# Performance work log

Measured on AMD Instinct MI355X. Metric: run time of the kernel, lower is better.

The kernel has to match this reference:

```python
import jax, jax.numpy as jnp
import numpy as np

EMBED = 1024
HEADS = 16
HEAD_DIM = EMBED // HEADS
HIDDEN = 4096
EPS = 1e-5


def setup_inputs() -> dict:
    key = jax.random.key(0)
    ks = jax.random.split(key, 12)
    s = 0.02
    inp = {
        "x": jax.random.normal(ks[0], (2, 2048, EMBED), dtype=jnp.float32),
        "ln1_scale": jnp.ones((EMBED,), jnp.float32),
        "ln1_shift": jnp.zeros((EMBED,), jnp.float32),
        "ln2_scale": jnp.ones((EMBED,), jnp.float32),
        "ln2_shift": jnp.zeros((EMBED,), jnp.float32),
        "wq": jax.random.normal(ks[1], (EMBED, EMBED), jnp.float32) * s,
        "bq": jnp.zeros((EMBED,), jnp.float32),
        "wk": jax.random.normal(ks[2], (EMBED, EMBED), jnp.float32) * s,
        "bk": jnp.zeros((EMBED,), jnp.float32),
        "wv": jax.random.normal(ks[3], (EMBED, EMBED), jnp.float32) * s,
        "bv": jnp.zeros((EMBED,), jnp.float32),
        "wo": jax.random.normal(ks[4], (EMBED, EMBED), jnp.float32) * s,
        "bo": jnp.zeros((EMBED,), jnp.float32),
        "w1": jax.random.normal(ks[5], (EMBED, HIDDEN), jnp.float32) * s,
        "b1": jnp.zeros((HIDDEN,), jnp.float32),
        "w2": jax.random.normal(ks[6], (HIDDEN, EMBED), jnp.float32) * s,
        "b2": jnp.zeros((EMBED,), jnp.float32),
    }
    return inp


def _layernorm(x, scale, shift):
    mean = jnp.mean(x, axis=-1, keepdims=True)
    var = jnp.var(x, axis=-1, keepdims=True)
    return scale * (x - mean) * jax.lax.rsqrt(var + EPS) + shift


def _block(x, ln1_scale, ln1_shift, ln2_scale, ln2_shift,
           wq, bq, wk, bk, wv, bv, wo, bo, w1, b1, w2, b2):
    B, S, D = x.shape
    h = _layernorm(x, ln1_scale, ln1_shift)
    q = (h @ wq + bq).reshape(B, S, HEADS, HEAD_DIM).transpose(0, 2, 1, 3)
    k = (h @ wk + bk).reshape(B, S, HEADS, HEAD_DIM).transpose(0, 2, 1, 3)
    v = (h @ wv + bv).reshape(B, S, HEADS, HEAD_DIM).transpose(0, 2, 1, 3)
    # [B,H,S,S] eager attention scores, matching the reference exactly
    scores = jnp.einsum("bhqd,bhkd->bhqk", q, k) * (HEAD_DIM ** -0.5)
    causal = jnp.tril(jnp.ones((S, S), dtype=bool))
    scores = jnp.where(causal, scores, -jnp.inf)
    attn = jax.nn.softmax(scores, axis=-1)
    ctx = jnp.einsum("bhqk,bhkd->bhqd", attn, v)
    ctx = ctx.transpose(0, 2, 1, 3).reshape(B, S, D)
    x = x + (ctx @ wo + bo)
    h = _layernorm(x, ln2_scale, ln2_shift)
    h = jax.nn.gelu(h @ w1 + b1, approximate=False)
    x = x + (h @ w2 + b2)
    return x


def reference(x, ln1_scale, ln1_shift, ln2_scale, ln2_shift,
              wq, bq, wk, bk, wv, bv, wo, bo, w1, b1, w2, b2):
    return _block(x, ln1_scale, ln1_shift, ln2_scale, ln2_shift,
                  wq, bq, wk, bk, wv, bv, wo, bo, w1, b1, w2, b2)
```

## Files before the change

kernel.cpp:

```cpp
#include <hip/hip_runtime.h>


typedef __bf16 bf16x8_t __attribute__((ext_vector_type(8)));
typedef float f32x4_t __attribute__((ext_vector_type(4)));
typedef unsigned short u16x8 __attribute__((ext_vector_type(8)));

__device__ __forceinline__ unsigned short f2b(float f) {
    unsigned int u = __builtin_bit_cast(unsigned int, f);
    u += 0x7fffu + ((u >> 16) & 1u);
    return (unsigned short)(u >> 16);
}
__device__ __forceinline__ bf16x8_t as_bf(u16x8 v) {
    return __builtin_bit_cast(bf16x8_t, v);
}
__device__ __forceinline__ void store_out(float* p, float v) { *p = v; }
__device__ __forceinline__ void store_out(unsigned short* p, float v) { *p = f2b(v); }

__device__ __forceinline__ void glds16(const unsigned short* g, unsigned short* l) {
    __builtin_amdgcn_global_load_lds(
        (const __attribute__((address_space(1))) unsigned int*)g,
        (__attribute__((address_space(3))) unsigned int*)l, 16, 0, 0);
}

template <int N>
__device__ __forceinline__ void wait_vm() {
    asm volatile("s_waitcnt vmcnt(%0)" ::"i"(N) : "memory");
}

__global__ __launch_bounds__(256) void transpose_cast(
    const float* __restrict__ src, unsigned short* __restrict__ dst,
    int K, int N) {
    __shared__ float tile[32][33];
    const int k0 = blockIdx.x * 32, n0 = blockIdx.y * 32;
    const int c = threadIdx.x & 31, r8 = threadIdx.x >> 5;
#pragma unroll
    for (int i = 0; i < 4; i++) {
        const int r = r8 + i * 8;
        tile[r][c] = src[(size_t)(k0 + r) * N + n0 + c];
    }
    __syncthreads();
#pragma unroll
    for (int i = 0; i < 4; i++) {
        const int rr = r8 + i * 8;
        dst[(size_t)(n0 + rr) * K + k0 + c] = f2b(tile[c][rr]);
    }
}

__global__ __launch_bounds__(256) void transpose_cast4(
    const float* __restrict__ s0, const float* __restrict__ s1,
    const float* __restrict__ s2, const float* __restrict__ s3,
    unsigned short* __restrict__ wqkvt, unsigned short* __restrict__ wot) {
    __shared__ float tile[32][33];
    const int z = blockIdx.z;
    const float* src = (z == 0) ? s0 : (z == 1) ? s1 : (z == 2) ? s2 : s3;
    unsigned short* dst = (z < 3) ? wqkvt + ((size_t)z << 20) : wot;
    const int k0 = blockIdx.x * 32, n0 = blockIdx.y * 32;
    const int c = threadIdx.x & 31, r8 = threadIdx.x >> 5;
#pragma unroll
    for (int i = 0; i < 4; i++) {
        const int r = r8 + i * 8;
        tile[r][c] = src[(size_t)(k0 + r) * 1024 + n0 + c];
    }
    __syncthreads();
#pragma unroll
    for (int i = 0; i < 4; i++) {
        const int rr = r8 + i * 8;
        dst[(size_t)(n0 + rr) * 1024 + k0 + c] = f2b(tile[c][rr]);
    }
}

__global__ __launch_bounds__(256) void vtrans_kernel(
    const unsigned short* __restrict__ src, unsigned short* __restrict__ dst) {
    __shared__ unsigned short tile[32][34];
    const int s0 = blockIdx.x * 32, hd0 = blockIdx.y * 32, b = blockIdx.z;
    const int c = threadIdx.x & 31, r8 = threadIdx.x >> 5;
#pragma unroll
    for (int i = 0; i < 4; i++) {
        const int r = r8 + i * 8;
        tile[r][c] = src[(size_t)(b * 2048 + s0 + r) * 3072 + hd0 + c];
    }
    __syncthreads();
#pragma unroll
    for (int i = 0; i < 4; i++) {
        const int rr = r8 + i * 8;
        dst[(size_t)(b * 1024 + hd0 + rr) * 2048 + s0 + c] = tile[c][rr];
    }
}

__global__ __launch_bounds__(256) void ln_kernel(
    const float* __restrict__ X,
    const float* __restrict__ scale,
    const float* __restrict__ shift,
    unsigned short* __restrict__ Hout) {
    const int tok = blockIdx.x;
    const int tid = threadIdx.x;
    const size_t base = (size_t)tok * 1024 + tid * 4;
    float4 xv = *(const float4*)(X + base);
    float f[4] = {xv.x, xv.y, xv.z, xv.w};
    float s = 0.f, s2 = 0.f;
#pragma unroll
    for (int i = 0; i < 4; i++) { s += f[i]; s2 += f[i] * f[i]; }
#pragma unroll
    for (int off = 32; off >= 1; off >>= 1) {
        s += __shfl_down(s, off);
        s2 += __shfl_down(s2, off);
    }
    __shared__ float red[8];
    const int wv = tid >> 6;
    if ((tid & 63) == 0) { red[wv] = s; red[4 + wv] = s2; }
    __syncthreads();
    s = red[0] + red[1] + red[2] + red[3];
    s2 = red[4] + red[5] + red[6] + red[7];
    const float mean = s * (1.f / 1024.f);
    const float var = s2 * (1.f / 1024.f) - mean * mean;
    const float rstd = rsqrtf(var + 1e-5f);
    const float4 sc = *(const float4*)(scale + tid * 4);
    const float4 sh = *(const float4*)(shift + tid * 4);
    unsigned short ov[4];
    ov[0] = f2b((f[0] - mean) * rstd * sc.x + sh.x);
    ov[1] = f2b((f[1] - mean) * rstd * sc.y + sh.y);
    ov[2] = f2b((f[2] - mean) * rstd * sc.z + sh.z);
    ov[3] = f2b((f[3] - mean) * rstd * sc.w + sh.w);
    *(unsigned long long*)(Hout + base) = *(unsigned long long*)ov;
}

template <int BN, int EPI, typename OutT>
__global__ __launch_bounds__(256) void gemm_kernel(
    const unsigned short* __restrict__ A, const unsigned short* __restrict__ Bt,
    const float* __restrict__ bp0, const float* __restrict__ bp1,
    const float* __restrict__ bp2, const float* __restrict__ bp3,
    const float* __restrict__ res, OutT* __restrict__ C, int M, int N, int K) {
    constexpr int BSUB = BN / 16;
    constexpr int JF = BN / 32;
    __shared__ __align__(16) unsigned short As[2][8 * 512];
    __shared__ __align__(16) unsigned short Bs[2][BSUB * 512];
    const int tid = threadIdx.x;
    const int w = tid >> 6, lane = tid & 63;
    const int quad = lane >> 4, l16 = lane & 15;
    const int bm = blockIdx.x * 128, bn = blockIdx.y * BN;
    const int wm = (w & 1) * 64, wn = (w >> 1) * (BN / 2);

    f32x4_t acc[4][JF];
#pragma unroll
    for (int i = 0; i < 4; i++)
#pragma unroll
        for (int j = 0; j < JF; j++) acc[i][j] = f32x4_t{0.f, 0.f, 0.f, 0.f};

    const unsigned short* Abase = A + (size_t)(bm + l16) * K + quad * 8;
    const unsigned short* Bbase = Bt + (size_t)(bn + l16) * K + quad * 8;

    {
        for (int s = w; s < 8; s += 4)
            glds16(Abase + (size_t)s * 16 * K, &As[0][s * 512]);
        for (int s = w; s < BSUB; s += 4)
            glds16(Bbase + (size_t)s * 16 * K, &Bs[0][s * 512]);
    }
    __syncthreads();

    int buf = 0;
    for (int k0 = 0; k0 < K; k0 += 32) {
        if (k0 + 32 < K) {
            const int kn = k0 + 32;
            for (int s = w; s < 8; s += 4)
                glds16(Abase + (size_t)s * 16 * K + kn, &As[buf ^ 1][s * 512]);
            for (int s = w; s < BSUB; s += 4)
                glds16(Bbase + (size_t)s * 16 * K + kn, &Bs[buf ^ 1][s * 512]);
        }
        bf16x8_t af[4], bfv[JF];
#pragma unroll
        for (int i = 0; i < 4; i++)
            af[i] = as_bf(*(const u16x8*)&As[buf][((wm >> 4) + i) * 512 + lane * 8]);
#pragma unroll
        for (int j = 0; j < JF; j++)
            bfv[j] = as_bf(*(const u16x8*)&Bs[buf][((wn >> 4) + j) * 512 + lane * 8]);
#pragma unroll
        for (int i = 0; i < 4; i++)
#pragma unroll
            for (int j = 0; j < JF; j++)
                acc[i][j] = __builtin_amdgcn_mfma_f32_16x16x32_bf16(af[i], bfv[j], acc[i][j], 0, 0, 0);
        __syncthreads();
        buf ^= 1;
    }

#pragma unroll
    for (int i = 0; i < 4; i++) {
        const int row = bm + wm + i * 16 + quad * 4;
#pragma unroll
        for (int j = 0; j < JF; j++) {
            const int col = bn + wn + j * 16 + l16;
            const int sel = col >> 10;
            const float* bp = (sel == 0) ? bp0 : (sel == 1) ? bp1 : (sel == 2) ? bp2 : bp3;
            const float bv = bp[col & 1023];
#pragma unroll
            for (int r = 0; r < 4; r++) {
                float v = acc[i][j][r] + bv;
                if (EPI == 1) v += res[(size_t)(row + r) * N + col];
                if (EPI == 2) v = 0.5f * v * (1.f + erff(v * 0.70710678118f));
                store_out(&C[(size_t)(row + r) * N + col], v);
            }
        }
    }
}

template <int EPI, typename OutT>
__global__ __launch_bounds__(512, 2) void gemm_pipe256(
    const unsigned short* __restrict__ A, const unsigned short* __restrict__ Bt,
    const float* __restrict__ bp0, const float* __restrict__ bp1,
    const float* __restrict__ bp2, const float* __restrict__ bp3,
    OutT* __restrict__ C, int M, int N, int K) {
    constexpr int D = 3, NBUF = 4;
    __shared__ __align__(16) unsigned short As[NBUF][16 * 512];
    __shared__ __align__(16) unsigned short Bs[NBUF][16 * 512];
    const int tid = threadIdx.x;
    const int w = tid >> 6, lane = tid & 63;
    const int quad = lane >> 4, l16 = lane & 15;
    const int bm = blockIdx.x * 256, bn = blockIdx.y * 256;
    const int wm = (w & 1) * 128, wn = (w >> 1) * 64;

    f32x4_t acc[8][4];
#pragma unroll
    for (int i = 0; i < 8; i++)
#pragma unroll
        for (int j = 0; j < 4; j++) acc[i][j] = f32x4_t{0.f, 0.f, 0.f, 0.f};

    const unsigned short* Abase = A + (size_t)(bm + l16) * K + quad * 8;
    const unsigned short* Bbase = Bt + (size_t)(bn + l16) * K + quad * 8;

    auto stage = [&](int kt, int bufi) {
        const int kn = kt * 32;
        const int s0 = w * 2, s1 = w * 2 + 1;
        glds16(Abase + (size_t)s0 * 16 * K + kn, &As[bufi][s0 * 512]);
        glds16(Abase + (size_t)s1 * 16 * K + kn, &As[bufi][s1 * 512]);
        glds16(Bbase + (size_t)s0 * 16 * K + kn, &Bs[bufi][s0 * 512]);
        glds16(Bbase + (size_t)s1 * 16 * K + kn, &Bs[bufi][s1 * 512]);
    };
    auto compute = [&](int bufi) {
        bf16x8_t af[8], bfv[4];
#pragma unroll
        for (int i = 0; i < 8; i++)
            af[i] = as_bf(*(const u16x8*)&As[bufi][((wm >> 4) + i) * 512 + lane * 8]);
#pragma unroll
        for (int j = 0; j < 4; j++)
            bfv[j] = as_bf(*(const u16x8*)&Bs[bufi][((wn >> 4) + j) * 512 + lane * 8]);
#pragma unroll
        for (int i = 0; i < 8; i++)
#pragma unroll
            for (int j = 0; j < 4; j++)
                acc[i][j] = __builtin_amdgcn_mfma_f32_16x16x32_bf16(af[i], bfv[j], acc[i][j], 0, 0, 0);
    };

    const int NT = K >> 5;
#pragma unroll
    for (int t = 0; t < D; ++t) stage(t, t);

    int buf = 0, sbuf = D;
    for (int t = 0; t < NT - D; ++t) {
        wait_vm<8>();
        __builtin_amdgcn_s_barrier();
        __builtin_amdgcn_sched_barrier(0);
        stage(t + D, sbuf);
        sbuf = (sbuf + 1) & 3;
        compute(buf);
        buf = (buf + 1) & 3;
    }
    wait_vm<8>(); __builtin_amdgcn_s_barrier(); __builtin_amdgcn_sched_barrier(0);
    compute(buf); buf = (buf + 1) & 3;
    wait_vm<4>(); __builtin_amdgcn_s_barrier(); __builtin_amdgcn_sched_barrier(0);
    compute(buf); buf = (buf + 1) & 3;
    wait_vm<0>(); __builtin_amdgcn_s_barrier(); __builtin_amdgcn_sched_barrier(0);
    compute(buf);

#pragma unroll
    for (int i = 0; i < 8; i++) {
        const int row = bm + wm + i * 16 + quad * 4;
#pragma unroll
        for (int j = 0; j < 4; j++) {
            const int col = bn + wn + j * 16 + l16;
            const int sel = col >> 10;
            const float* bp = (sel == 0) ? bp0 : (sel == 1) ? bp1 : (sel == 2) ? bp2 : bp3;
            const float bv = bp[col & 1023];
#pragma unroll
            for (int r = 0; r < 4; r++) {
                float v = acc[i][j][r] + bv;
                if (EPI == 2) v = 0.5f * v * (1.f + erff(v * 0.70710678118f));
                store_out(&C[(size_t)(row + r) * N + col], v);
            }
        }
    }
}

#define LP 68

__global__ __launch_bounds__(256, 3) void attn_kernel(
    const unsigned short* __restrict__ Q, const unsigned short* __restrict__ K,
    const unsigned short* __restrict__ Vt, unsigned short* __restrict__ O,
    int ld) {
    __shared__ __align__(16) unsigned short Ks[2][8 * 512];
    __shared__ __align__(16) unsigned short Vs[2][8 * 512];
    __shared__ __align__(16) unsigned short Ps[4][32 * LP];
    const int tid = threadIdx.x;
    const int w = tid >> 6, lane = tid & 63;
    const int quad = lane >> 4, l16 = lane & 15;
    const int hh = blockIdx.x >> 1, bb = blockIdx.x & 1;
    const int y = blockIdx.y;
    const int qb = (y >= 8) ? (y - 8) : (15 - y);
    const int q0 = qb * 128;
    const int tmax = 2 * qb + 1;
    const size_t seqbase = (size_t)bb * 2048;
    const int hoff = hh * 64;
    const unsigned short* vtb = Vt + (size_t)(bb * 16 + hh) * 64 * 2048;
    const float cs = 0.18033688f;

    bf16x8_t qf[2][2];
#pragma unroll
    for (int i = 0; i < 2; i++) {
        const unsigned short* qr = Q + (seqbase + q0 + i * 64 + w * 16 + l16) * ld + hoff;
        qf[i][0] = as_bf(*(const u16x8*)(qr + quad * 8));
        qf[i][1] = as_bf(*(const u16x8*)(qr + 32 + quad * 8));
    }

    f32x4_t o[2][4];
#pragma unroll
    for (int i = 0; i < 2; i++)
#pragma unroll
        for (int jd = 0; jd < 4; jd++) o[i][jd] = f32x4_t{0.f, 0.f, 0.f, 0.f};
    float ls[2][4] = {{0.f, 0.f, 0.f, 0.f}, {0.f, 0.f, 0.f, 0.f}};

    auto stage = [&](int t, int buf) {
        for (int s = w; s < 16; s += 4) {
            if (s < 8) {
                const unsigned short* src =
                    K + (seqbase + t * 64 + (s >> 1) * 16 + l16) * ld + hoff + (s & 1) * 32 + quad * 8;
                glds16(src, &Ks[buf][s * 512]);
            } else {
                const int v = s - 8;
                const unsigned short* src =
                    vtb + (size_t)((v >> 1) * 16 + l16) * 2048 + t * 64 + (v & 1) * 32 + quad * 8;
                glds16(src, &Vs[buf][v * 512]);
            }
        }
    };

    stage(0, 0);
    __syncthreads();

    int buf = 0;
    for (int t = 0; t <= tmax; ++t) {
        if (t < tmax) stage(t + 1, buf ^ 1);

        bf16x8_t kf[4][2], vf[4][2];
#pragma unroll
        for (int jn = 0; jn < 4; jn++) {
            kf[jn][0] = as_bf(*(const u16x8*)&Ks[buf][(jn * 2 + 0) * 512 + lane * 8]);
            kf[jn][1] = as_bf(*(const u16x8*)&Ks[buf][(jn * 2 + 1) * 512 + lane * 8]);
            vf[jn][0] = as_bf(*(const u16x8*)&Vs[buf][(jn * 2 + 0) * 512 + lane * 8]);
            vf[jn][1] = as_bf(*(const u16x8*)&Vs[buf][(jn * 2 + 1) * 512 + lane * 8]);
        }

#pragma unroll
        for (int i = 0; i < 2; i++) {
            if (i == 0 && t > 2 * qb) continue;
            const bool diag = (t == 2 * qb + i);
#pragma unroll
            for (int jn = 0; jn < 4; jn++) {
                f32x4_t z = f32x4_t{0.f, 0.f, 0.f, 0.f};
                z = __builtin_amdgcn_mfma_f32_16x16x32_bf16(qf[i][0], kf[jn][0], z, 0, 0, 0);
                z = __builtin_amdgcn_mfma_f32_16x16x32_bf16(qf[i][1], kf[jn][1], z, 0, 0, 0);
#pragma unroll
                for (int r = 0; r < 4; r++) {
                    float p = exp2f(fminf(z[r] * cs, 60.f));
                    if (diag) {
                        const int col = t * 64 + jn * 16 + l16;
                        const int row = q0 + i * 64 + w * 16 + quad * 4 + r;
                        p = (col <= row) ? p : 0.f;
                    }
                    ls[i][r] += p;
                    Ps[w][(i * 16 + quad * 4 + r) * LP + jn * 16 + l16] = f2b(p);
                }
            }
        }

#pragma unroll
        for (int i = 0; i < 2; i++) {
            if (i == 0 && t > 2 * qb) continue;
            const bf16x8_t pf0 = as_bf(*(const u16x8*)&Ps[w][(i * 16 + l16) * LP + quad * 8]);
            const bf16x8_t pf1 = as_bf(*(const u16x8*)&Ps[w][(i * 16 + l16) * LP + 32 + quad * 8]);
#pragma unroll
            for (int jd = 0; jd < 4; jd++) {
                o[i][jd] = __builtin_amdgcn_mfma_f32_16x16x32_bf16(pf0, vf[jd][0], o[i][jd], 0, 0, 0);
                o[i][jd] = __builtin_amdgcn_mfma_f32_16x16x32_bf16(pf1, vf[jd][1], o[i][jd], 0, 0, 0);
            }
        }
        __syncthreads();
        buf ^= 1;
    }

#pragma unroll
    for (int i = 0; i < 2; i++)
#pragma unroll
        for (int r = 0; r < 4; r++) {
            float s = ls[i][r];
            s += __shfl_xor(s, 1);
            s += __shfl_xor(s, 2);
            s += __shfl_xor(s, 4);
            s += __shfl_xor(s, 8);
            const float inv = 1.f / s;
            const size_t row = seqbase + q0 + i * 64 + w * 16 + quad * 4 + r;
#pragma unroll
            for (int jd = 0; jd < 4; jd++)
                O[row * 1024 + hoff + jd * 16 + l16] = f2b(o[i][jd][r] * inv);
        }
}

extern "C" void kernel_launch(void* const* d_in, const int* in_sizes, int n_in,
                              void* d_out, int out_size, void* d_ws, size_t ws_size,
                              hipStream_t stream) {
    const float* x = (const float*)d_in[0];
    const float* ln1s = (const float*)d_in[1];
    const float* ln1b = (const float*)d_in[2];
    const float* ln2s = (const float*)d_in[3];
    const float* ln2b = (const float*)d_in[4];
    const float* wq = (const float*)d_in[5];
    const float* bq = (const float*)d_in[6];
    const float* wk = (const float*)d_in[7];
    const float* bk = (const float*)d_in[8];
    const float* wv = (const float*)d_in[9];
    const float* bv = (const float*)d_in[10];
    const float* wo = (const float*)d_in[11];
    const float* bo = (const float*)d_in[12];
    const float* w1 = (const float*)d_in[13];
    const float* b1 = (const float*)d_in[14];
    const float* w2 = (const float*)d_in[15];
    const float* b2 = (const float*)d_in[16];
    float* out = (float*)d_out;

    char* ws = (char*)d_ws;
    const size_t MB = 1u << 20;
    unsigned short* wqkvt = (unsigned short*)(ws + 0 * MB);
    unsigned short* wot   = (unsigned short*)(ws + 6 * MB);
    unsigned short* w1t   = (unsigned short*)(ws + 8 * MB);
    unsigned short* w2t   = (unsigned short*)(ws + 16 * MB);
    unsigned short* h     = (unsigned short*)(ws + 24 * MB);
    unsigned short* vt    = (unsigned short*)(ws + 24 * MB);
    unsigned short* qkv   = (unsigned short*)(ws + 32 * MB);
    unsigned short* ctx   = (unsigned short*)(ws + 56 * MB);
    unsigned short* h2    = (unsigned short*)(ws + 24 * MB);
    float*          x1    = (float*)(ws + 64 * MB);
    unsigned short* g     = (unsigned short*)(ws + 32 * MB);

    const dim3 blk(256);

    transpose_cast4<<<dim3(32, 32, 4), blk, 0, stream>>>(wq, wk, wv, wo, wqkvt, wot);
    transpose_cast<<<dim3(32, 128), blk, 0, stream>>>(w1, w1t, 1024, 4096);
    transpose_cast<<<dim3(128, 32), blk, 0, stream>>>(w2, w2t, 4096, 1024);

    ln_kernel<<<4096, blk, 0, stream>>>(x, ln1s, ln1b, h);
    gemm_pipe256<0, unsigned short><<<dim3(16, 12), dim3(512), 0, stream>>>(
        h, wqkvt, bq, bk, bv, bv, qkv, 4096, 3072, 1024);
    vtrans_kernel<<<dim3(64, 32, 2), blk, 0, stream>>>(qkv + 2048, vt);
    attn_kernel<<<dim3(32, 16), blk, 0, stream>>>(qkv, qkv + 1024, vt, ctx, 3072);
    gemm_kernel<64, 1, float><<<dim3(32, 16), blk, 0, stream>>>(
        ctx, wot, bo, bo, bo, bo, x, x1, 4096, 1024, 1024);
    ln_kernel<<<4096, blk, 0, stream>>>(x1, ln2s, ln2b, h2);
    gemm_pipe256<2, unsigned short><<<dim3(16, 16), dim3(512), 0, stream>>>(
        h2, w1t, b1, b1 + 1024, b1 + 2048, b1 + 3072, g, 4096, 4096, 1024);
    gemm_kernel<64, 1, float><<<dim3(32, 16), blk, 0, stream>>>(
        g, w2t, b2, b2, b2, b2, x1, out, 4096, 1024, 4096);
}
```

Measured before the change: 486.9 us.

## Replace N=1024 GEMMs with split-K 256-tile pipeline using atomic accumulation

```diff
diff --git a/kernel.cpp b/kernel.cpp
--- a/kernel.cpp
+++ b/kernel.cpp
@@ -124,82 +124,16 @@
     *(unsigned long long*)(Hout + base) = *(unsigned long long*)ov;
 }
 
-template <int BN, int EPI, typename OutT>
-__global__ __launch_bounds__(256) void gemm_kernel(
-    const unsigned short* __restrict__ A, const unsigned short* __restrict__ Bt,
-    const float* __restrict__ bp0, const float* __restrict__ bp1,
-    const float* __restrict__ bp2, const float* __restrict__ bp3,
-    const float* __restrict__ res, OutT* __restrict__ C, int M, int N, int K) {
-    constexpr int BSUB = BN / 16;
-    constexpr int JF = BN / 32;
-    __shared__ __align__(16) unsigned short As[2][8 * 512];
-    __shared__ __align__(16) unsigned short Bs[2][BSUB * 512];
-    const int tid = threadIdx.x;
-    const int w = tid >> 6, lane = tid & 63;
-    const int quad = lane >> 4, l16 = lane & 15;
-    const int bm = blockIdx.x * 128, bn = blockIdx.y * BN;
-    const int wm = (w & 1) * 64, wn = (w >> 1) * (BN / 2);
-
-    f32x4_t acc[4][JF];
-#pragma unroll
-    for (int i = 0; i < 4; i++)
-#pragma unroll
-        for (int j = 0; j < JF; j++) acc[i][j] = f32x4_t{0.f, 0.f, 0.f, 0.f};
-
-    const unsigned short* Abase = A + (size_t)(bm + l16) * K + quad * 8;
-    const unsigned short* Bbase = Bt + (size_t)(bn + l16) * K + quad * 8;
-
-    {
-        for (int s = w; s < 8; s += 4)
-            glds16(Abase + (size_t)s * 16 * K, &As[0][s * 512]);
-        for (int s = w; s < BSUB; s += 4)
-            glds16(Bbase + (size_t)s * 16 * K, &Bs[0][s * 512]);
-    }
-    __syncthreads();
-
-    int buf = 0;
-    for (int k0 = 0; k0 < K; k0 += 32) {
-        if (k0 + 32 < K) {
-            const int kn = k0 + 32;
-            for (int s = w; s < 8; s += 4)
-                glds16(Abase + (size_t)s * 16 * K + kn, &As[buf ^ 1][s * 512]);
-            for (int s = w; s < BSUB; s += 4)
-                glds16(Bbase + (size_t)s * 16 * K + kn, &Bs[buf ^ 1][s * 512]);
-        }
-        bf16x8_t af[4], bfv[JF];
-#pragma unroll
-        for (int i = 0; i < 4; i++)
-            af[i] = as_bf(*(const u16x8*)&As[buf][((wm >> 4) + i) * 512 + lane * 8]);
-#pragma unroll
-        for (int j = 0; j < JF; j++)
-            bfv[j] = as_bf(*(const u16x8*)&Bs[buf][((wn >> 4) + j) * 512 + lane * 8]);
-#pragma unroll
-        for (int i = 0; i < 4; i++)
-#pragma unroll
-            for (int j = 0; j < JF; j++)
-                acc[i][j] = __builtin_amdgcn_mfma_f32_16x16x32_bf16(af[i], bfv[j], acc[i][j], 0, 0, 0);
-        __syncthreads();
-        buf ^= 1;
-    }
-
-#pragma unroll
-    for (int i = 0; i < 4; i++) {
-        const int row = bm + wm + i * 16 + quad * 4;
-#pragma unroll
-        for (int j = 0; j < JF; j++) {
-            const int col = bn + wn + j * 16 + l16;
-            const int sel = col >> 10;
-            const float* bp = (sel == 0) ? bp0 : (sel == 1) ? bp1 : (sel == 2) ? bp2 : bp3;
-            const float bv = bp[col & 1023];
-#pragma unroll
-            for (int r = 0; r < 4; r++) {
-                float v = acc[i][j][r] + bv;
-                if (EPI == 1) v += res[(size_t)(row + r) * N + col];
-                if (EPI == 2) v = 0.5f * v * (1.f + erff(v * 0.70710678118f));
-                store_out(&C[(size_t)(row + r) * N + col], v);
-            }
-        }
-    }
+__global__ __launch_bounds__(256) void bias_res_init(
+    const float* __restrict__ res, const float* __restrict__ bias,
+    float* __restrict__ out) {
+    const size_t i = (size_t)blockIdx.x * 256 + threadIdx.x;
+    const int col4 = (int)(i & 255);
+    const float4 r = ((const float4*)res)[i];
+    const float4 b = ((const float4*)bias)[col4];
+    float4 o;
+    o.x = r.x + b.x; o.y = r.y + b.y; o.z = r.z + b.z; o.w = r.w + b.w;
+    ((float4*)out)[i] = o;
 }
 
 template <int EPI, typename OutT>
@@ -207,7 +141,7 @@
     const unsigned short* __restrict__ A, const unsigned short* __restrict__ Bt,
     const float* __restrict__ bp0, const float* __restrict__ bp1,
     const float* __restrict__ bp2, const float* __restrict__ bp3,
-    OutT* __restrict__ C, int M, int N, int K) {
+    OutT* __restrict__ C, int M, int N, int K, int Ko) {
     constexpr int D = 3, NBUF = 4;
     __shared__ __align__(16) unsigned short As[NBUF][16 * 512];
     __shared__ __align__(16) unsigned short Bs[NBUF][16 * 512];
@@ -215,6 +149,7 @@
     const int w = tid >> 6, lane = tid & 63;
     const int quad = lane >> 4, l16 = lane & 15;
     const int bm = blockIdx.x * 256, bn = blockIdx.y * 256;
+    const int kz = blockIdx.z;
     const int wm = (w & 1) * 128, wn = (w >> 1) * 64;
 
     f32x4_t acc[8][4];
@@ -223,8 +158,8 @@
 #pragma unroll
         for (int j = 0; j < 4; j++) acc[i][j] = f32x4_t{0.f, 0.f, 0.f, 0.f};
 
-    const unsigned short* Abase = A + (size_t)(bm + l16) * K + quad * 8;
-    const unsigned short* Bbase = Bt + (size_t)(bn + l16) * K + quad * 8;
+    const unsigned short* Abase = A + (size_t)(bm + l16) * K + (size_t)kz * Ko + quad * 8;
+    const unsigned short* Bbase = Bt + (size_t)(bn + l16) * K + (size_t)kz * Ko + quad * 8;
 
     auto stage = [&](int kt, int bufi) {
         const int kn = kt * 32;
@@ -249,7 +184,7 @@
                 acc[i][j] = __builtin_amdgcn_mfma_f32_16x16x32_bf16(af[i], bfv[j], acc[i][j], 0, 0, 0);
     };
 
-    const int NT = K >> 5;
+    const int NT = Ko >> 5;
 #pragma unroll
     for (int t = 0; t < D; ++t) stage(t, t);
 
@@ -276,14 +211,21 @@
 #pragma unroll
         for (int j = 0; j < 4; j++) {
             const int col = bn + wn + j * 16 + l16;
-            const int sel = col >> 10;
-            const float* bp = (sel == 0) ? bp0 : (sel == 1) ? bp1 : (sel == 2) ? bp2 : bp3;
-            const float bv = bp[col & 1023];
-#pragma unroll
-            for (int r = 0; r < 4; r++) {
-                float v = acc[i][j][r] + bv;
-                if (EPI == 2) v = 0.5f * v * (1.f + erff(v * 0.70710678118f));
-                store_out(&C[(size_t)(row + r) * N + col], v);
+            if constexpr (EPI == 3) {
+#pragma unroll
+                for (int r = 0; r < 4; r++)
+                    atomicAdd(reinterpret_cast<float*>(&C[(size_t)(row + r) * N + col]),
+                              acc[i][j][r]);
+            } else {
+                const int sel = col >> 10;
+                const float* bp = (sel == 0) ? bp0 : (sel == 1) ? bp1 : (sel == 2) ? bp2 : bp3;
+                const float bv = bp[col & 1023];
+#pragma unroll
+                for (int r = 0; r < 4; r++) {
+                    float v = acc[i][j][r] + bv;
+                    if (EPI == 2) v = 0.5f * v * (1.f + erff(v * 0.70710678118f));
+                    store_out(&C[(size_t)(row + r) * N + col], v);
+                }
             }
         }
     }
@@ -456,14 +398,16 @@
 
     ln_kernel<<<4096, blk, 0, stream>>>(x, ln1s, ln1b, h);
     gemm_pipe256<0, unsigned short><<<dim3(16, 12), dim3(512), 0, stream>>>(
-        h, wqkvt, bq, bk, bv, bv, qkv, 4096, 3072, 1024);
+        h, wqkvt, bq, bk, bv, bv, qkv, 4096, 3072, 1024, 1024);
     vtrans_kernel<<<dim3(64, 32, 2), blk, 0, stream>>>(qkv + 2048, vt);
     attn_kernel<<<dim3(32, 16), blk, 0, stream>>>(qkv, qkv + 1024, vt, ctx, 3072);
-    gemm_kernel<64, 1, float><<<dim3(32, 16), blk, 0, stream>>>(
-        ctx, wot, bo, bo, bo, bo, x, x1, 4096, 1024, 1024);
+    bias_res_init<<<4096, blk, 0, stream>>>(x, bo, x1);
+    gemm_pipe256<3, float><<<dim3(16, 4, 4), dim3(512), 0, stream>>>(
+        ctx, wot, bo, bo, bo, bo, x1, 4096, 1024, 1024, 256);
     ln_kernel<<<4096, blk, 0, stream>>>(x1, ln2s, ln2b, h2);
     gemm_pipe256<2, unsigned short><<<dim3(16, 16), dim3(512), 0, stream>>>(
-        h2, w1t, b1, b1 + 1024, b1 + 2048, b1 + 3072, g, 4096, 4096, 1024);
-    gemm_kernel<64, 1, float><<<dim3(32, 16), blk, 0, stream>>>(
-        g, w2t, b2, b2, b2, b2, x1, out, 4096, 1024, 4096);
-}
+        h2, w1t, b1, b1 + 1024, b1 + 2048, b1 + 3072, g, 4096, 4096, 1024, 1024);
+    bias_res_init<<<4096, blk, 0, stream>>>(x1, b2, out);
+    gemm_pipe256<3, float><<<dim3(16, 4, 4), dim3(512), 0, stream>>>(
+        g, w2t, b2, b2, b2, b2, out, 4096, 1024, 4096, 1024);
+}
```

After: 535.7 us. +10.0%, slower.
